# Optimization experiments

Hardware: AMD Instinct MI355X
Metric: run time of the kernel (lower is better)

## Reference

```python
import jax, jax.numpy as jnp
import numpy as np

H, I, E, K = 1024, 2048, 8, 2
B, T = 4, 2048


def setup_inputs() -> dict:
    key = jax.random.key(0)
    k0, k1, k2, k3 = jax.random.split(key, 4)
    x = jax.random.normal(k0, (B, T, H), dtype=jnp.float32)
    Wg = jax.random.normal(k1, (E, H), dtype=jnp.float32) * 0.02   # gate: Linear(H->E), weight [E,H]
    W1 = jax.random.normal(k2, (E, I, H), dtype=jnp.float32) * 0.02  # per-expert fc1 weights [I,H]
    W2 = jax.random.normal(k3, (E, H, I), dtype=jnp.float32) * 0.02  # per-expert fc2 weights [H,I]
    return {"x": x, "Wg": Wg, "W1": W1, "W2": W2, "top_k": K}


def reference(x, Wg, W1, W2, top_k):
    b, t, h = x.shape
    xf = x.reshape(-1, h)                                  # [N,H], N=B*T
    gate_probs = jax.nn.softmax(xf @ Wg.T, axis=-1)        # [N,E]
    topk_vals, topk_idx = jax.lax.top_k(gate_probs, top_k) # [N,k]
    # Dense all-expert SiLU-MLP (faithful to the original dense MoE):
    hid = jax.nn.silu(jnp.einsum('nh,eih->nei', xf, W1))   # [N,E,I]
    all_outs = jnp.einsum('nei,ehi->neh', hid, W2)         # [N,E,H]
    topk_outs = jnp.take_along_axis(all_outs, topk_idx[:, :, None], axis=1)  # [N,k,H]
    weighted = (topk_outs * topk_vals[:, :, None]).sum(axis=1)               # [N,H]
    return weighted.reshape(b, t, h)
```

## Files before the change

kernel.cpp:

```cpp
#include <hip/hip_runtime.h>
#include <hip/hip_bf16.h>

#define HH 1024
#define II 2048
#define EE 8
#define NTOK 8192
#define NPAIR (NTOK * 2)

typedef __attribute__((ext_vector_type(8))) short bf16x8;
typedef __attribute__((ext_vector_type(4))) float f32x4;
typedef unsigned int u32;

__device__ __forceinline__ ushort f2bf(float f) {
    union { float f; unsigned u; } v; v.f = f;
    unsigned r = v.u + 0x7fffu + ((v.u >> 16) & 1u);
    return (ushort)(r >> 16);
}

__device__ __forceinline__ void gload16(const void* g, void* l) {
    __builtin_amdgcn_global_load_lds((const __attribute__((address_space(1))) u32*)g,
                                     (__attribute__((address_space(3))) u32*)l, 16, 0, 0);
}

__global__ __launch_bounds__(256) void cvtw_kernel(
    const float* __restrict__ W1, const float* __restrict__ W2,
    ushort* __restrict__ W1b, ushort* __restrict__ W2b)
{
    const int N1 = EE * II * HH / 4;
    const int i = blockIdx.x * 256 + threadIdx.x;
    const float4 f = (i < N1) ? ((const float4*)W1)[i] : ((const float4*)W2)[i - N1];
    union { ushort h[4]; uint2 u; } pk;
    pk.h[0] = f2bf(f.x); pk.h[1] = f2bf(f.y); pk.h[2] = f2bf(f.z); pk.h[3] = f2bf(f.w);
    if (i < N1) ((uint2*)W1b)[i] = pk.u;
    else        ((uint2*)W2b)[i - N1] = pk.u;
}

__global__ __launch_bounds__(256) void gate_kernel(
    const float* __restrict__ x, const float* __restrict__ Wg,
    int* __restrict__ counts, int* __restrict__ tki, float* __restrict__ tkv,
    ushort* __restrict__ xb)
{
    __shared__ int hist[EE];
    const int tid = threadIdx.x;
    if (tid < EE) hist[tid] = 0;
    __syncthreads();

    const int w = tid >> 6, lane = tid & 63;

#pragma unroll 1
    for (int t = 0; t < 8; t++) {
        const int n = blockIdx.x * 32 + w * 8 + t;
        const float* xr = x + (size_t)n * HH;
        float4 xv[4];
#pragma unroll
        for (int c = 0; c < 4; c++) xv[c] = *(const float4*)(xr + c * 256 + lane * 4);

#pragma unroll
        for (int c = 0; c < 4; c++) {
            union { ushort h[4]; uint2 u; } pk;
            pk.h[0] = f2bf(xv[c].x); pk.h[1] = f2bf(xv[c].y);
            pk.h[2] = f2bf(xv[c].z); pk.h[3] = f2bf(xv[c].w);
            *(uint2*)(xb + (size_t)n * HH + c * 256 + lane * 4) = pk.u;
        }

        float dot[EE];
#pragma unroll
        for (int e = 0; e < EE; e++) {
            float s = 0.f;
#pragma unroll
            for (int c = 0; c < 4; c++) {
                const float4 wv = *(const float4*)(Wg + e * HH + c * 256 + lane * 4);
                s += xv[c].x * wv.x + xv[c].y * wv.y + xv[c].z * wv.z + xv[c].w * wv.w;
            }
            for (int off = 32; off > 0; off >>= 1) s += __shfl_down(s, off);
            dot[e] = s;
        }
        if (lane == 0) {
            float m = dot[0];
#pragma unroll
            for (int e = 1; e < EE; e++) m = fmaxf(m, dot[e]);
            float p[EE]; float sum = 0.f;
#pragma unroll
            for (int e = 0; e < EE; e++) { p[e] = __expf(dot[e] - m); sum += p[e]; }
            const float inv = 1.f / sum;
            int i0 = 0; float v0 = p[0];
#pragma unroll
            for (int e = 1; e < EE; e++) if (p[e] > v0) { v0 = p[e]; i0 = e; }
            int i1 = -1; float v1 = -1.f;
#pragma unroll
            for (int e = 0; e < EE; e++) if (e != i0 && p[e] > v1) { v1 = p[e]; i1 = e; }
            tki[n * 2 + 0] = i0; tkv[n * 2 + 0] = v0 * inv;
            tki[n * 2 + 1] = i1; tkv[n * 2 + 1] = v1 * inv;
            atomicAdd(&hist[i0], 1);
            atomicAdd(&hist[i1], 1);
        }
    }
    __syncthreads();
    if (tid < EE) atomicAdd(&counts[tid], hist[tid]);
}

__global__ void offsets_kernel(const int* __restrict__ counts,
                               int* __restrict__ offs, int* __restrict__ cursor)
{
    if (threadIdx.x == 0 && blockIdx.x == 0) {
        int acc = 0;
        for (int e = 0; e < EE; e++) { offs[e] = acc; cursor[e] = acc; acc += counts[e]; }
    }
}

__global__ __launch_bounds__(256) void scatter_kernel(
    const int* __restrict__ tki, const float* __restrict__ tkv,
    int* __restrict__ cursor, int* __restrict__ stok, float* __restrict__ sval)
{
    __shared__ int hist[EE];
    __shared__ int base[EE];
    const int tid = threadIdx.x;
    const int id = blockIdx.x * 256 + tid;
    if (tid < EE) hist[tid] = 0;
    __syncthreads();
    const int e = tki[id];
    const int loc = atomicAdd(&hist[e], 1);
    __syncthreads();
    if (tid < EE) base[tid] = atomicAdd(&cursor[tid], hist[tid]);
    __syncthreads();
    const int p = base[e] + loc;
    stok[p] = id >> 1;
    sval[p] = tkv[id];
}

template <bool PRE>
__global__ __launch_bounds__(256) void fc1_kernel(
    const float* __restrict__ x, const ushort* __restrict__ xb,
    const float* __restrict__ W1, const ushort* __restrict__ W1b,
    const int* __restrict__ counts, const int* __restrict__ offs,
    const int* __restrict__ stok, ushort* __restrict__ hid)
{
    const int e = blockIdx.z;
    const int cnt = counts[e];
    const int row0 = blockIdx.y * 128;
    if (row0 >= cnt) return;
    const int off = offs[e];
    const int col0 = blockIdx.x * 128;

    __shared__ __align__(16) ushort As[128 * 64];
    __shared__ __align__(16) ushort Bs[128 * 64];

    const int tid = threadIdx.x;
    const int w = tid >> 6, lane = tid & 63;
    const int quad = lane >> 4, l16 = lane & 15;
    const int wm = (w >> 1) * 64, wn = (w & 1) * 64;
    const int l7 = l16 & 7;

    f32x4 acc[4][4];
#pragma unroll
    for (int mi = 0; mi < 4; mi++)
#pragma unroll
        for (int ni = 0; ni < 4; ni++) acc[mi][ni] = f32x4{0.f, 0.f, 0.f, 0.f};

    const int sub = lane >> 3;
    const int chk = lane & 7;
    const int gchk = chk ^ sub;
    int tokA[4];
    const int fr = tid >> 1;
    const int fc = (tid & 1) * 32;
    int tokF = 0;
    if (PRE) {
#pragma unroll
        for (int i = 0; i < 4; i++) {
            int r = row0 + (w * 4 + i) * 8 + sub;
            if (r >= cnt) r = cnt - 1;
            tokA[i] = stok[off + r];
        }
    } else {
        int r = row0 + fr;
        if (r >= cnt) r = cnt - 1;
        tokF = stok[off + r];
    }

    for (int k0 = 0; k0 < HH; k0 += 64) {
        __syncthreads();
        if (PRE) {
#pragma unroll
            for (int i = 0; i < 4; i++) {
                const ushort* gA = xb + (size_t)tokA[i] * HH + k0 + gchk * 8;
                gload16(gA, &As[(w * 4 + i) * 512]);
                const ushort* gB = W1b + ((size_t)e * II + col0 + (w * 4 + i) * 8 + sub) * HH + k0 + gchk * 8;
                gload16(gB, &Bs[(w * 4 + i) * 512]);
            }
        } else {
#pragma unroll
            for (int c = 0; c < 32; c += 4) {
                const int u = fc + c;
                const int sw = ((u >> 3) ^ (fr & 7)) * 8 + (u & 7);
                const float4 f = *(const float4*)(x + (size_t)tokF * HH + k0 + u);
                union { ushort h[4]; uint2 u2; } pk;
                pk.h[0] = f2bf(f.x); pk.h[1] = f2bf(f.y); pk.h[2] = f2bf(f.z); pk.h[3] = f2bf(f.w);
                *(uint2*)&As[fr * 64 + sw] = pk.u2;
                const float4 g = *(const float4*)(W1 + ((size_t)e * II + col0 + fr) * HH + k0 + u);
                pk.h[0] = f2bf(g.x); pk.h[1] = f2bf(g.y); pk.h[2] = f2bf(g.z); pk.h[3] = f2bf(g.w);
                *(uint2*)&Bs[fr * 64 + sw] = pk.u2;
            }
        }
        __syncthreads();

#pragma unroll
        for (int kk = 0; kk < 2; kk++) {
            const int pos = ((kk * 4 + quad) ^ l7) * 8;
            bf16x8 af[4], bb[4];
#pragma unroll
            for (int mi = 0; mi < 4; mi++)
                af[mi] = *(const bf16x8*)&As[(wm + mi * 16 + l16) * 64 + pos];
#pragma unroll
            for (int ni = 0; ni < 4; ni++)
                bb[ni] = *(const bf16x8*)&Bs[(wn + ni * 16 + l16) * 64 + pos];
#pragma unroll
            for (int mi = 0; mi < 4; mi++)
#pragma unroll
                for (int ni = 0; ni < 4; ni++)
                    acc[mi][ni] = __builtin_amdgcn_mfma_f32_16x16x32_bf16(af[mi], bb[ni], acc[mi][ni], 0, 0, 0);
        }
    }

    const int cnt_rem = cnt - row0;
#pragma unroll
    for (int mi = 0; mi < 4; mi++) {
#pragma unroll
        for (int j = 0; j < 4; j++) {
            const int r = wm + mi * 16 + quad * 4 + j;
            if (r < cnt_rem) {
                ushort* hrow = hid + (size_t)(off + row0 + r) * II + col0 + wn + l16;
#pragma unroll
                for (int ni = 0; ni < 4; ni++) {
                    const float v = acc[mi][ni][j];
                    const float s = v / (1.f + __expf(-v));
                    hrow[ni * 16] = f2bf(s);
                }
            }
        }
    }
}

template <bool PRE>
__global__ __launch_bounds__(256) void fc2_kernel(
    const ushort* __restrict__ hid,
    const float* __restrict__ W2, const ushort* __restrict__ W2b,
    const int* __restrict__ counts, const int* __restrict__ offs,
    const int* __restrict__ stok, const float* __restrict__ sval,
    float* __restrict__ out)
{
    const int e = blockIdx.z;
    const int cnt = counts[e];
    const int row0 = blockIdx.y * 128;
    if (row0 >= cnt) return;
    const int off = offs[e];
    const int col0 = blockIdx.x * 128;

    __shared__ __align__(16) ushort As[128 * 64];
    __shared__ __align__(16) ushort Bs[128 * 64];

    const int tid = threadIdx.x;
    const int w = tid >> 6, lane = tid & 63;
    const int quad = lane >> 4, l16 = lane & 15;
    const int wm = (w >> 1) * 64, wn = (w & 1) * 64;
    const int l7 = l16 & 7;

    f32x4 acc[4][4];
#pragma unroll
    for (int mi = 0; mi < 4; mi++)
#pragma unroll
        for (int ni = 0; ni < 4; ni++) acc[mi][ni] = f32x4{0.f, 0.f, 0.f, 0.f};

    const int sub = lane >> 3;
    const int chk = lane & 7;
    const int gchk = chk ^ sub;
    size_t slotA[4];
#pragma unroll
    for (int i = 0; i < 4; i++) {
        int s = off + row0 + (w * 4 + i) * 8 + sub;
        if (s > NPAIR - 1) s = NPAIR - 1;
        slotA[i] = (size_t)s;
    }
    const int fr = tid >> 1;
    const int fc = (tid & 1) * 32;

    for (int k0 = 0; k0 < II; k0 += 64) {
        __syncthreads();
#pragma unroll
        for (int i = 0; i < 4; i++) {
            const ushort* gA = hid + slotA[i] * II + k0 + gchk * 8;
            gload16(gA, &As[(w * 4 + i) * 512]);
        }
        if (PRE) {
#pragma unroll
            for (int i = 0; i < 4; i++) {
                const ushort* gB = W2b + ((size_t)e * HH + col0 + (w * 4 + i) * 8 + sub) * II + k0 + gchk * 8;
                gload16(gB, &Bs[(w * 4 + i) * 512]);
            }
        } else {
#pragma unroll
            for (int c = 0; c < 32; c += 4) {
                const int u = fc + c;
                const int sw = ((u >> 3) ^ (fr & 7)) * 8 + (u & 7);
                const float4 g = *(const float4*)(W2 + ((size_t)e * HH + col0 + fr) * II + k0 + u);
                union { ushort h[4]; uint2 u2; } pk;
                pk.h[0] = f2bf(g.x); pk.h[1] = f2bf(g.y); pk.h[2] = f2bf(g.z); pk.h[3] = f2bf(g.w);
                *(uint2*)&Bs[fr * 64 + sw] = pk.u2;
            }
        }
        __syncthreads();

#pragma unroll
        for (int kk = 0; kk < 2; kk++) {
            const int pos = ((kk * 4 + quad) ^ l7) * 8;
            bf16x8 af[4], bb[4];
#pragma unroll
            for (int mi = 0; mi < 4; mi++)
                af[mi] = *(const bf16x8*)&As[(wm + mi * 16 + l16) * 64 + pos];
#pragma unroll
            for (int ni = 0; ni < 4; ni++)
                bb[ni] = *(const bf16x8*)&Bs[(wn + ni * 16 + l16) * 64 + pos];
#pragma unroll
            for (int mi = 0; mi < 4; mi++)
#pragma unroll
                for (int ni = 0; ni < 4; ni++)
                    acc[mi][ni] = __builtin_amdgcn_mfma_f32_16x16x32_bf16(af[mi], bb[ni], acc[mi][ni], 0, 0, 0);
        }
    }

    const int cnt_rem = cnt - row0;
#pragma unroll
    for (int mi = 0; mi < 4; mi++) {
#pragma unroll
        for (int j = 0; j < 4; j++) {
            const int r = wm + mi * 16 + quad * 4 + j;
            if (r < cnt_rem) {
                const int p = off + row0 + r;
                const int token = stok[p];
                const float val = sval[p];
                float* orow = out + (size_t)token * HH + col0 + wn + l16;
#pragma unroll
                for (int ni = 0; ni < 4; ni++)
                    atomicAdd(&orow[ni * 16], val * acc[mi][ni][j]);
            }
        }
    }
}

extern "C" void kernel_launch(void* const* d_in, const int* in_sizes, int n_in,
                              void* d_out, int out_size, void* d_ws, size_t ws_size,
                              hipStream_t stream) {
    const float* x  = (const float*)d_in[0];
    const float* Wg = (const float*)d_in[1];
    const float* W1 = (const float*)d_in[2];
    const float* W2 = (const float*)d_in[3];
    float* out = (float*)d_out;

    char* wsb = (char*)d_ws;
    int*    counts = (int*)(wsb + 0);
    int*    cursor = (int*)(wsb + 64);
    int*    offs   = (int*)(wsb + 128);
    int*    tki    = (int*)(wsb + 256);
    float*  tkv    = (float*)(wsb + 256 + 65536);
    int*    stok   = (int*)(wsb + 256 + 2 * 65536);
    float*  sval   = (float*)(wsb + 256 + 3 * 65536);
    ushort* hid    = (ushort*)(wsb + 262400);
    ushort* W1b    = (ushort*)(wsb + 262400 + 67108864ull);
    ushort* W2b    = (ushort*)(wsb + 262400 + 100663296ull);
    ushort* xb     = (ushort*)(wsb + 262400 + 134217728ull);
    const size_t REQ = 262400ull + 134217728ull + 16777216ull;
    const bool pre = ws_size >= REQ;

    hipMemsetAsync(wsb, 0, 256, stream);
    hipMemsetAsync(d_out, 0, (size_t)out_size * sizeof(float), stream);

    gate_kernel<<<NTOK / 32, 256, 0, stream>>>(x, Wg, counts, tki, tkv, xb);
    offsets_kernel<<<1, 64, 0, stream>>>(counts, offs, cursor);
    scatter_kernel<<<NPAIR / 256, 256, 0, stream>>>(tki, tkv, cursor, stok, sval);

    if (pre) {
        cvtw_kernel<<<(2 * EE * II * HH / 4) / 256, 256, 0, stream>>>(W1, W2, W1b, W2b);
        fc1_kernel<true><<<dim3(II / 128, NPAIR / 128, EE), 256, 0, stream>>>(x, xb, W1, W1b, counts, offs, stok, hid);
        fc2_kernel<true><<<dim3(HH / 128, NPAIR / 128, EE), 256, 0, stream>>>(hid, W2, W2b, counts, offs, stok, sval, out);
    } else {
        fc1_kernel<false><<<dim3(II / 128, NPAIR / 128, EE), 256, 0, stream>>>(x, xb, W1, W1b, counts, offs, stok, hid);
        fc2_kernel<false><<<dim3(HH / 128, NPAIR / 128, EE), 256, 0, stream>>>(hid, W2, W2b, counts, offs, stok, sval, out);
    }
}
```

Before: 479.7 us.

## Double-buffer LDS tiles in fc1/fc2 pre-converted paths to overlap loads with MFMA

In the bf16 pre-converted (PRE) paths of both expert GEMM kernels, the shared-memory A/B tiles become two ping-pong buffers. The next K-tile's async global-to-LDS loads are issued right after the barrier and before the MFMA work on the current tile, so load latency can hide behind compute. This also drops one barrier per iteration. The cost is twice the LDS per block, which may reduce how many blocks fit on a CU. The non-PRE fallback keeps its old single-buffer behaviour using buffer 0.

```diff
diff --git a/kernel.cpp b/kernel.cpp
--- a/kernel.cpp
+++ b/kernel.cpp
@@ -142,8 +142,8 @@
     const int off = offs[e];
     const int col0 = blockIdx.x * 128;
 
-    __shared__ __align__(16) ushort As[128 * 64];
-    __shared__ __align__(16) ushort Bs[128 * 64];
+    __shared__ __align__(16) ushort As[2][128 * 64];
+    __shared__ __align__(16) ushort Bs[2][128 * 64];
 
     const int tid = threadIdx.x;
     const int w = tid >> 6, lane = tid & 63;
@@ -177,17 +177,44 @@
         tokF = stok[off + r];
     }
 
-    for (int k0 = 0; k0 < HH; k0 += 64) {
-        __syncthreads();
-        if (PRE) {
+    if (PRE) {
+        auto issue = [&](int buf, int k0) {
 #pragma unroll
             for (int i = 0; i < 4; i++) {
                 const ushort* gA = xb + (size_t)tokA[i] * HH + k0 + gchk * 8;
-                gload16(gA, &As[(w * 4 + i) * 512]);
+                gload16(gA, &As[buf][(w * 4 + i) * 512]);
                 const ushort* gB = W1b + ((size_t)e * II + col0 + (w * 4 + i) * 8 + sub) * HH + k0 + gchk * 8;
-                gload16(gB, &Bs[(w * 4 + i) * 512]);
-            }
-        } else {
+                gload16(gB, &Bs[buf][(w * 4 + i) * 512]);
+            }
+        };
+        issue(0, 0);
+        const int ITERS = HH / 64;
+#pragma unroll 1
+        for (int it = 0; it < ITERS; it++) {
+            const int cur = it & 1;
+            __syncthreads();
+            if (it + 1 < ITERS) issue(1 - cur, (it + 1) * 64);
+#pragma unroll
+            for (int kk = 0; kk < 2; kk++) {
+                const int pos = ((kk * 4 + quad) ^ l7) * 8;
+                bf16x8 af[4], bb[4];
+#pragma unroll
+                for (int mi = 0; mi < 4; mi++)
+                    af[mi] = *(const bf16x8*)&As[cur][(wm + mi * 16 + l16) * 64 + pos];
+#pragma unroll
+                for (int ni = 0; ni < 4; ni++)
+                    bb[ni] = *(const bf16x8*)&Bs[cur][(wn + ni * 16 + l16) * 64 + pos];
+#pragma unroll
+                for (int mi = 0; mi < 4; mi++)
+#pragma unroll
+                    for (int ni = 0; ni < 4; ni++)
+                        acc[mi][ni] = __builtin_amdgcn_mfma_f32_16x16x32_bf16(af[mi], bb[ni], acc[mi][ni], 0, 0, 0);
+            }
+        }
+    } else {
+#pragma unroll 1
+        for (int k0 = 0; k0 < HH; k0 += 64) {
+            __syncthreads();
 #pragma unroll
             for (int c = 0; c < 32; c += 4) {
                 const int u = fc + c;
@@ -195,29 +222,28 @@
                 const float4 f = *(const float4*)(x + (size_t)tokF * HH + k0 + u);
                 union { ushort h[4]; uint2 u2; } pk;
                 pk.h[0] = f2bf(f.x); pk.h[1] = f2bf(f.y); pk.h[2] = f2bf(f.z); pk.h[3] = f2bf(f.w);
-                *(uint2*)&As[fr * 64 + sw] = pk.u2;
+                *(uint2*)&As[0][fr * 64 + sw] = pk.u2;
                 const float4 g = *(const float4*)(W1 + ((size_t)e * II + col0 + fr) * HH + k0 + u);
                 pk.h[0] = f2bf(g.x); pk.h[1] = f2bf(g.y); pk.h[2] = f2bf(g.z); pk.h[3] = f2bf(g.w);
-                *(uint2*)&Bs[fr * 64 + sw] = pk.u2;
-            }
-        }
-        __syncthreads();
-
-#pragma unroll
-        for (int kk = 0; kk < 2; kk++) {
-            const int pos = ((kk * 4 + quad) ^ l7) * 8;
-            bf16x8 af[4], bb[4];
-#pragma unroll
-            for (int mi = 0; mi < 4; mi++)
-                af[mi] = *(const bf16x8*)&As[(wm + mi * 16 + l16) * 64 + pos];
-#pragma unroll
-            for (int ni = 0; ni < 4; ni++)
-                bb[ni] = *(const bf16x8*)&Bs[(wn + ni * 16 + l16) * 64 + pos];
-#pragma unroll
-            for (int mi = 0; mi < 4; mi++)
+                *(uint2*)&Bs[0][fr * 64 + sw] = pk.u2;
+            }
+            __syncthreads();
+#pragma unroll
+            for (int kk = 0; kk < 2; kk++) {
+                const int pos = ((kk * 4 + quad) ^ l7) * 8;
+                bf16x8 af[4], bb[4];
+#pragma unroll
+                for (int mi = 0; mi < 4; mi++)
+                    af[mi] = *(const bf16x8*)&As[0][(wm + mi * 16 + l16) * 64 + pos];
 #pragma unroll
                 for (int ni = 0; ni < 4; ni++)
-                    acc[mi][ni] = __builtin_amdgcn_mfma_f32_16x16x32_bf16(af[mi], bb[ni], acc[mi][ni], 0, 0, 0);
+                    bb[ni] = *(const bf16x8*)&Bs[0][(wn + ni * 16 + l16) * 64 + pos];
+#pragma unroll
+                for (int mi = 0; mi < 4; mi++)
+#pragma unroll
+                    for (int ni = 0; ni < 4; ni++)
+                        acc[mi][ni] = __builtin_amdgcn_mfma_f32_16x16x32_bf16(af[mi], bb[ni], acc[mi][ni], 0, 0, 0);
+            }
         }
     }
 
@@ -255,8 +281,8 @@
     const int off = offs[e];
     const int col0 = blockIdx.x * 128;
 
-    __shared__ __align__(16) ushort As[128 * 64];
-    __shared__ __align__(16) ushort Bs[128 * 64];
+    __shared__ __align__(16) ushort As[2][128 * 64];
+    __shared__ __align__(16) ushort Bs[2][128 * 64];
 
     const int tid = threadIdx.x;
     const int w = tid >> 6, lane = tid & 63;
@@ -283,20 +309,49 @@
     const int fr = tid >> 1;
     const int fc = (tid & 1) * 32;
 
-    for (int k0 = 0; k0 < II; k0 += 64) {
-        __syncthreads();
-#pragma unroll
-        for (int i = 0; i < 4; i++) {
-            const ushort* gA = hid + slotA[i] * II + k0 + gchk * 8;
-            gload16(gA, &As[(w * 4 + i) * 512]);
-        }
-        if (PRE) {
+    if (PRE) {
+        auto issue = [&](int buf, int k0) {
 #pragma unroll
             for (int i = 0; i < 4; i++) {
+                const ushort* gA = hid + slotA[i] * II + k0 + gchk * 8;
+                gload16(gA, &As[buf][(w * 4 + i) * 512]);
                 const ushort* gB = W2b + ((size_t)e * HH + col0 + (w * 4 + i) * 8 + sub) * II + k0 + gchk * 8;
-                gload16(gB, &Bs[(w * 4 + i) * 512]);
-            }
-        } else {
+                gload16(gB, &Bs[buf][(w * 4 + i) * 512]);
+            }
+        };
+        issue(0, 0);
+        const int ITERS = II / 64;
+#pragma unroll 1
+        for (int it = 0; it < ITERS; it++) {
+            const int cur = it & 1;
+            __syncthreads();
+            if (it + 1 < ITERS) issue(1 - cur, (it + 1) * 64);
+#pragma unroll
+            for (int kk = 0; kk < 2; kk++) {
+                const int pos = ((kk * 4 + quad) ^ l7) * 8;
+                bf16x8 af[4], bb[4];
+#pragma unroll
+                for (int mi = 0; mi < 4; mi++)
+                    af[mi] = *(const bf16x8*)&As[cur][(wm + mi * 16 + l16) * 64 + pos];
+#pragma unroll
+                for (int ni = 0; ni < 4; ni++)
+                    bb[ni] = *(const bf16x8*)&Bs[cur][(wn + ni * 16 + l16) * 64 + pos];
+#pragma unroll
+                for (int mi = 0; mi < 4; mi++)
+#pragma unroll
+                    for (int ni = 0; ni < 4; ni++)
+                        acc[mi][ni] = __builtin_amdgcn_mfma_f32_16x16x32_bf16(af[mi], bb[ni], acc[mi][ni], 0, 0, 0);
+            }
+        }
+    } else {
+#pragma unroll 1
+        for (int k0 = 0; k0 < II; k0 += 64) {
+            __syncthreads();
+#pragma unroll
+            for (int i = 0; i < 4; i++) {
+                const ushort* gA = hid + slotA[i] * II + k0 + gchk * 8;
+                gload16(gA, &As[0][(w * 4 + i) * 512]);
+            }
 #pragma unroll
             for (int c = 0; c < 32; c += 4) {
                 const int u = fc + c;
@@ -304,26 +359,25 @@
                 const float4 g = *(const float4*)(W2 + ((size_t)e * HH + col0 + fr) * II + k0 + u);
                 union { ushort h[4]; uint2 u2; } pk;
                 pk.h[0] = f2bf(g.x); pk.h[1] = f2bf(g.y); pk.h[2] = f2bf(g.z); pk.h[3] = f2bf(g.w);
-                *(uint2*)&Bs[fr * 64 + sw] = pk.u2;
-            }
-        }
-        __syncthreads();
-
-#pragma unroll
-        for (int kk = 0; kk < 2; kk++) {
-            const int pos = ((kk * 4 + quad) ^ l7) * 8;
-            bf16x8 af[4], bb[4];
-#pragma unroll
-            for (int mi = 0; mi < 4; mi++)
-                af[mi] = *(const bf16x8*)&As[(wm + mi * 16 + l16) * 64 + pos];
-#pragma unroll
-            for (int ni = 0; ni < 4; ni++)
-                bb[ni] = *(const bf16x8*)&Bs[(wn + ni * 16 + l16) * 64 + pos];
-#pragma unroll
-            for (int mi = 0; mi < 4; mi++)
+                *(uint2*)&Bs[0][fr * 64 + sw] = pk.u2;
+            }
+            __syncthreads();
+#pragma unroll
+            for (int kk = 0; kk < 2; kk++) {
+                const int pos = ((kk * 4 + quad) ^ l7) * 8;
+                bf16x8 af[4], bb[4];
+#pragma unroll
+                for (int mi = 0; mi < 4; mi++)
+                    af[mi] = *(const bf16x8*)&As[0][(wm + mi * 16 + l16) * 64 + pos];
 #pragma unroll
                 for (int ni = 0; ni < 4; ni++)
-                    acc[mi][ni] = __builtin_amdgcn_mfma_f32_16x16x32_bf16(af[mi], bb[ni], acc[mi][ni], 0, 0, 0);
+                    bb[ni] = *(const bf16x8*)&Bs[0][(wn + ni * 16 + l16) * 64 + pos];
+#pragma unroll
+                for (int mi = 0; mi < 4; mi++)
+#pragma unroll
+                    for (int ni = 0; ni < 4; ni++)
+                        acc[mi][ni] = __builtin_amdgcn_mfma_f32_16x16x32_bf16(af[mi], bb[ni], acc[mi][ni], 0, 0, 0);
+            }
         }
     }
 
```

After: 455.4 us. 1.05x faster.
